# Kernel tuning notes

Hardware: AMD Instinct MI355X
Metric: run time of the kernel (lower is better)

## Reference

```python
import jax, jax.numpy as jnp
import numpy as np

B, S, V, D = 64, 256, 50000, 300
NW, CL, CV, CD = 8192, 16, 500, 30
H, T, CH = 128, 17, 30


def setup_inputs() -> dict:
    key = jax.random.key(0)
    ks = jax.random.split(key, 32)
    f32 = jnp.float32
    def rn(k, shape, scale=0.1):
        return jax.random.normal(k, shape, dtype=f32) * scale
    inp = {}
    inp["char_emb"] = rn(ks[0], (CV, CD)).at[0].set(0.0)  # padding_idx=0
    inp["conv_w"] = rn(ks[1], (CH, CD, 3))  # OIH
    inp["conv_b"] = rn(ks[2], (CH,))
    inp["word_emb"] = rn(ks[3], (V, D))
    in0, in1 = D + CH, 2 * H
    inp["w_ih_l0"] = rn(ks[4], (2, 3 * H, in0))  # [dir, 3H, in]
    inp["w_hh_l0"] = rn(ks[5], (2, 3 * H, H))
    inp["b_ih_l0"] = rn(ks[6], (2, 3 * H))
    inp["b_hh_l0"] = rn(ks[7], (2, 3 * H))
    inp["w_ih_l1"] = rn(ks[8], (2, 3 * H, in1))
    inp["w_hh_l1"] = rn(ks[9], (2, 3 * H, H))
    inp["b_ih_l1"] = rn(ks[10], (2, 3 * H))
    inp["b_hh_l1"] = rn(ks[11], (2, 3 * H))
    inp["mlp_w1"] = rn(ks[12], (2 * H, H))
    inp["mlp_b1"] = rn(ks[13], (H,))
    inp["mlp_w2"] = rn(ks[14], (H, T))
    inp["mlp_b2"] = rn(ks[15], (T,))
    inp["crf_start"] = rn(ks[16], (T,))
    inp["crf_end"] = rn(ks[17], (T,))
    inp["crf_trans"] = rn(ks[18], (T, T))
    inp["batched_char_words"] = jax.random.randint(ks[19], (NW, CL), 0, CV)
    inp["batched_char_words_len"] = jax.random.randint(ks[20], (NW,), 1, CL + 1)
    inp["batched_char_word_index"] = jax.random.randint(ks[21], (B, S), 0, NW + 1)
    inp["batched_tokens"] = jax.random.randint(ks[22], (B, S), 0, V)
    inp["batched_tokens_len"] = jax.random.randint(ks[23], (B,), S // 2, S + 1)
    inp["target"] = jax.random.randint(ks[24], (B, S), 0, T)
    return inp


def _gru_dir(x, mask, w_ih, w_hh, b_ih, b_hh, reverse):
    # x: [B,S,I], mask: [B,S] bool. Masked (padded) steps carry hidden state
    # through unchanged, matching pack_padded_sequence semantics.
    xg = jnp.einsum('bsi,gi->sbg', x, w_ih) + b_ih  # [S,B,3H]
    m = mask.T  # [S,B]
    h0 = jnp.zeros((x.shape[0], w_hh.shape[1]), x.dtype)

    def step(h, inp):
        xt, mt = inp
        hg = h @ w_hh.T + b_hh
        xr, xz, xn = jnp.split(xt, 3, axis=-1)
        hr, hz, hn = jnp.split(hg, 3, axis=-1)
        r = jax.nn.sigmoid(xr + hr)
        z = jax.nn.sigmoid(xz + hz)
        n = jnp.tanh(xn + r * hn)
        hnew = (1.0 - z) * n + z * h
        h = jnp.where(mt[:, None], hnew, h)
        return h, h

    _, hs = jax.lax.scan(step, h0, (xg, m), reverse=reverse)
    return hs.transpose(1, 0, 2)  # [B,S,H]


def _bigru_layer(x, mask, w_ih, w_hh, b_ih, b_hh):
    fwd = _gru_dir(x, mask, w_ih[0], w_hh[0], b_ih[0], b_hh[0], False)
    bwd = _gru_dir(x, mask, w_ih[1], w_hh[1], b_ih[1], b_hh[1], True)
    return jnp.concatenate([fwd, bwd], axis=-1)


def _forward(char_emb, conv_w, conv_b, word_emb,
             w_ih_l0, w_hh_l0, b_ih_l0, b_hh_l0,
             w_ih_l1, w_hh_l1, b_ih_l1, b_hh_l1,
             mlp_w1, mlp_b1, mlp_w2, mlp_b2,
             crf_start, crf_end, crf_trans,
             batched_char_words, batched_char_word_index,
             batched_tokens, batched_tokens_len, target):
    # --- char CNN token encoder: conv1d(k=3, SAME) + relu + max-over-time ---
    ct = char_emb[batched_char_words]  # [NW,CL,CD]
    c = jax.lax.conv_general_dilated(ct.transpose(0, 2, 1), conv_w, (1,), 'SAME',
                                     dimension_numbers=('NCH', 'OIH', 'NCH'))
    c = jax.nn.relu(c + conv_b[None, :, None])
    tok_enc = jnp.max(c, axis=-1)  # [NW,CH]
    tok_enc = jnp.concatenate([jnp.zeros((1, tok_enc.shape[1]), tok_enc.dtype), tok_enc], axis=0)
    tok_idx = tok_enc[batched_char_word_index]  # [B,S,CH] (index 0 -> zeros)

    texts = jnp.concatenate([word_emb[batched_tokens], tok_idx], axis=-1)  # [B,S,D+CH]
    seq = batched_tokens.shape[1]
    mask = jnp.arange(seq)[None, :] < batched_tokens_len[:, None]  # [B,S]

    # --- 2-layer BiGRU ---
    h = _bigru_layer(texts, mask, w_ih_l0, w_hh_l0, b_ih_l0, b_hh_l0)
    h = _bigru_layer(h, mask, w_ih_l1, w_hh_l1, b_ih_l1, b_hh_l1)

    # --- MLP head -> emissions [B,S,17] ---
    h = jax.nn.relu(h @ mlp_w1 + mlp_b1)
    emissions = h @ mlp_w2 + mlp_b2

    # --- CRF negative log-likelihood, reduction='token_mean' ---
    maskf = mask.astype(emissions.dtype)
    emit_sc = jnp.take_along_axis(emissions, target[..., None], axis=-1)[..., 0]  # [B,S]
    trans_sc = crf_trans[target[:, :-1], target[:, 1:]]  # [B,S-1]
    score = crf_start[target[:, 0]] + emit_sc[:, 0]
    score = score + jnp.sum((trans_sc + emit_sc[:, 1:]) * maskf[:, 1:], axis=1)
    last_tags = jnp.take_along_axis(target, (batched_tokens_len - 1)[:, None], axis=1)[:, 0]
    score = score + crf_end[last_tags]

    alpha0 = crf_start[None, :] + emissions[:, 0]  # [B,T]
    em_rest = emissions[:, 1:].transpose(1, 0, 2)  # [S-1,B,T]
    m_rest = mask[:, 1:].T  # [S-1,B]

    def crf_step(alpha, inp):
        emit, mt = inp
        new = jax.nn.logsumexp(alpha[:, :, None] + crf_trans[None], axis=1) + emit
        return jnp.where(mt[:, None], new, alpha), None

    alpha, _ = jax.lax.scan(crf_step, alpha0, (em_rest, m_rest))
    log_z = jax.nn.logsumexp(alpha + crf_end[None, :], axis=1)
    llh = score - log_z
    return -(jnp.sum(llh) / jnp.sum(maskf))


def reference(char_emb, conv_w, conv_b, word_emb,
              w_ih_l0, w_hh_l0, b_ih_l0, b_hh_l0,
              w_ih_l1, w_hh_l1, b_ih_l1, b_hh_l1,
              mlp_w1, mlp_b1, mlp_w2, mlp_b2,
              crf_start, crf_end, crf_trans,
              batched_char_words, batched_char_words_len,
              batched_char_word_index, batched_tokens, batched_tokens_len, target):
    return _forward(char_emb, conv_w, conv_b, word_emb,
                    w_ih_l0, w_hh_l0, b_ih_l0, b_hh_l0,
                    w_ih_l1, w_hh_l1, b_ih_l1, b_hh_l1,
                    mlp_w1, mlp_b1, mlp_w2, mlp_b2,
                    crf_start, crf_end, crf_trans,
                    batched_char_words, batched_char_word_index,
                    batched_tokens, batched_tokens_len, target)
```

## Files before the change

kernel.cpp:

```cpp
#include <hip/hip_runtime.h>
#include <cstddef>

#define BATCH 64
#define SEQ   256
#define VOCAB 50000
#define DIM   300
#define NW    8192
#define CLEN  16
#define CDIM  30
#define CHC   30
#define HID   128
#define NT    17
#define IN0   (DIM + CHC)
#define IN0P  336
#define IN1   (2 * HID)
#define NPOS  (BATCH * SEQ)

constexpr size_t SZ_XG    = 2ull * BATCH * SEQ * 384;
constexpr size_t SZ_TEXTS = (size_t)NPOS * IN0P;
constexpr size_t SZ_H1    = (size_t)NPOS * 256;
constexpr size_t SZ_TOK   = 245792;
constexpr size_t SZ_EMIS  = (size_t)NPOS * NT;
constexpr size_t SZ_WPAD  = 768ull * IN0P;
constexpr size_t OFF_XG    = 0;
constexpr size_t OFF_TEXTS = OFF_XG + SZ_XG;
constexpr size_t OFF_H1    = OFF_TEXTS + SZ_TEXTS;
constexpr size_t OFF_TOK   = OFF_H1 + SZ_H1;
constexpr size_t OFF_EMIS  = OFF_TOK + SZ_TOK;
constexpr size_t OFF_WPAD  = OFF_EMIS + SZ_EMIS;
constexpr size_t OFF_LLH   = OFF_WPAD + SZ_WPAD;

__device__ __forceinline__ float sigm(float x) {
    return 1.f / (1.f + __expf(-x));
}
__device__ __forceinline__ float tanh_fast(float x) {
    x = fminf(fmaxf(x, -15.f), 15.f);
    float e = __expf(-2.f * x);
    return (1.f - e) / (1.f + e);
}
__device__ __forceinline__ float oct_sum(float x) {
    int y = __builtin_amdgcn_update_dpp(0, __float_as_int(x), 0xB1, 0xF, 0xF, false);
    x += __int_as_float(y);
    y = __builtin_amdgcn_update_dpp(0, __float_as_int(x), 0x4E, 0xF, 0xF, false);
    x += __int_as_float(y);
    y = __builtin_amdgcn_update_dpp(0, __float_as_int(x), 0x141, 0xF, 0xF, false);
    x += __int_as_float(y);
    return x;
}

__global__ __launch_bounds__(256) void char_conv_k(
    const float* __restrict__ char_emb,
    const float* __restrict__ conv_w,
    const float* __restrict__ conv_b,
    const int*   __restrict__ words,
    float* __restrict__ tok_enc)
{
    __shared__ __align__(16) float cs[8][CLEN][CDIM];
    __shared__ float wsm[CHC * CDIM * 3];
    __shared__ float bs[CHC];
    int n0 = blockIdx.x * 8;
    int tid = threadIdx.x;
    for (int e = tid; e < CHC * CDIM * 3; e += 256) wsm[e] = conv_w[e];
    if (tid < CHC) bs[tid] = conv_b[tid];
    for (int e = tid; e < 8 * CLEN * CDIM; e += 256) {
        int wi = e / (CLEN * CDIM);
        int rem = e - wi * (CLEN * CDIM);
        int l = rem / CDIM;
        int i = rem - l * CDIM;
        int ci = words[(n0 + wi) * CLEN + l];
        cs[wi][l][i] = char_emb[ci * CDIM + i];
    }
    __syncthreads();
    int wi = tid >> 5;
    int o = tid & 31;
    if (o < CHC) {
        float best = -1e30f;
        for (int l = 0; l < CLEN; l++) {
            float s = 0.f;
            #pragma unroll
            for (int k = 0; k < 3; k++) {
                int ll = l + k - 1;
                if (ll >= 0 && ll < CLEN) {
                    #pragma unroll
                    for (int i = 0; i < CDIM; i++)
                        s += cs[wi][ll][i] * wsm[(o * CDIM + i) * 3 + k];
                }
            }
            best = fmaxf(best, s);
        }
        tok_enc[(size_t)(n0 + wi + 1) * CDIM + o] = fmaxf(best + bs[o], 0.f);
    }
}

__global__ __launch_bounds__(128) void build_texts_k(
    const float* __restrict__ word_emb,
    const float* __restrict__ tok_enc,
    const int*   __restrict__ tokens,
    const int*   __restrict__ widx,
    float* __restrict__ texts)
{
    int p = blockIdx.x;
    int tok = tokens[p];
    int ci = widx[p];
    float* o = texts + (size_t)p * IN0P;
    const float* wr = word_emb + (size_t)tok * DIM;
    const float* tr = tok_enc + (size_t)ci * CDIM;
    for (int c = threadIdx.x; c < IN0P; c += 128)
        o[c] = (c < DIM) ? wr[c] : (c < IN0 ? tr[c - DIM] : 0.f);
}

__global__ __launch_bounds__(64) void pad_w_k(
    const float* __restrict__ w, float* __restrict__ wp)
{
    int r = blockIdx.x;
    for (int c = threadIdx.x; c < IN0P; c += 64)
        wp[(size_t)r * IN0P + c] = (c < IN0) ? w[(size_t)r * IN0 + c] : 0.f;
}

#define GBM 128
#define GBN 128
#define GBK 16
__global__ __launch_bounds__(256) void gemm_xg_k(
    const float* __restrict__ A,
    const float* __restrict__ W,
    const float* __restrict__ bias,
    float* __restrict__ out,
    int K)
{
    __shared__ __align__(16) float As[GBK][GBM];
    __shared__ __align__(16) float Ws[GBK][GBN];
    int tid = threadIdx.x;
    int m0 = blockIdx.x * GBM;
    int n0 = blockIdx.y * GBN;
    int lrow = tid >> 1;
    int lk = (tid & 1) * 8;
    int ty = tid >> 4;
    int tx = tid & 15;

    float acc[8][8];
    #pragma unroll
    for (int i = 0; i < 8; i++)
        #pragma unroll
        for (int j = 0; j < 8; j++) acc[i][j] = 0.f;

    for (int k0 = 0; k0 < K; k0 += GBK) {
        const float4* ap = (const float4*)(A + (size_t)(m0 + lrow) * K + k0 + lk);
        const float4* wp = (const float4*)(W + (size_t)(n0 + lrow) * K + k0 + lk);
        float4 va0 = ap[0], va1 = ap[1];
        float4 vw0 = wp[0], vw1 = wp[1];
        As[lk + 0][lrow] = va0.x; As[lk + 1][lrow] = va0.y;
        As[lk + 2][lrow] = va0.z; As[lk + 3][lrow] = va0.w;
        As[lk + 4][lrow] = va1.x; As[lk + 5][lrow] = va1.y;
        As[lk + 6][lrow] = va1.z; As[lk + 7][lrow] = va1.w;
        Ws[lk + 0][lrow] = vw0.x; Ws[lk + 1][lrow] = vw0.y;
        Ws[lk + 2][lrow] = vw0.z; Ws[lk + 3][lrow] = vw0.w;
        Ws[lk + 4][lrow] = vw1.x; Ws[lk + 5][lrow] = vw1.y;
        Ws[lk + 6][lrow] = vw1.z; Ws[lk + 7][lrow] = vw1.w;
        __syncthreads();
        #pragma unroll
        for (int k = 0; k < GBK; k++) {
            float4 a0 = *(const float4*)&As[k][ty * 8];
            float4 a1 = *(const float4*)&As[k][ty * 8 + 4];
            float4 b0 = *(const float4*)&Ws[k][tx * 8];
            float4 b1 = *(const float4*)&Ws[k][tx * 8 + 4];
            float av[8] = {a0.x, a0.y, a0.z, a0.w, a1.x, a1.y, a1.z, a1.w};
            float bv[8] = {b0.x, b0.y, b0.z, b0.w, b1.x, b1.y, b1.z, b1.w};
            #pragma unroll
            for (int i = 0; i < 8; i++)
                #pragma unroll
                for (int j = 0; j < 8; j++)
                    acc[i][j] += av[i] * bv[j];
        }
        __syncthreads();
    }
    int nb = n0 + tx * 8;
    int d = nb / 384;
    int g0 = nb - d * 384;
    float bvv[8];
    #pragma unroll
    for (int j = 0; j < 8; j++) bvv[j] = bias[nb + j];
    int mbase = m0 + ty * 8;
    #pragma unroll
    for (int i = 0; i < 8; i++) {
        int m = mbase + i;
        int b = m >> 8;
        int t = m & 255;
        float* op = out + (((size_t)(d * BATCH + b) * SEQ + t) * 384 + g0);
        #pragma unroll
        for (int j = 0; j < 8; j++) op[j] = acc[i][j] + bvv[j];
    }
}

__global__ __launch_bounds__(512, 1) void gru_rec_k(
    const float* __restrict__ xg,
    const float* __restrict__ w_hh,
    const float* __restrict__ b_hh,
    const int*   __restrict__ lens,
    float* __restrict__ out)
{
    int d = blockIdx.x & 1;
    int b = blockIdx.x >> 1;
    int i = threadIdx.x;
    int e0 = i >> 3;
    int e1 = e0 + 64;
    int c = i & 7;
    __shared__ __align__(16) float hS[2][HID];

    const float* wb = w_hh + (size_t)d * 384 * HID;
    float4 wR0[4], wZ0[4], wN0[4], wR1[4], wZ1[4], wN1[4];
    #pragma unroll
    for (int q = 0; q < 4; q++) {
        int m = (q + c) & 3;
        int off = 16 * c + 4 * m;
        wR0[q] = *(const float4*)(wb + (size_t)(e0)       * HID + off);
        wZ0[q] = *(const float4*)(wb + (size_t)(128 + e0) * HID + off);
        wN0[q] = *(const float4*)(wb + (size_t)(256 + e0) * HID + off);
        wR1[q] = *(const float4*)(wb + (size_t)(e1)       * HID + off);
        wZ1[q] = *(const float4*)(wb + (size_t)(128 + e1) * HID + off);
        wN1[q] = *(const float4*)(wb + (size_t)(256 + e1) * HID + off);
    }
    float bhR0 = b_hh[d * 384 + e0];
    float bhZ0 = b_hh[d * 384 + 128 + e0];
    float bhN0 = b_hh[d * 384 + 256 + e0];
    float bhR1 = b_hh[d * 384 + e1];
    float bhZ1 = b_hh[d * 384 + 128 + e1];
    float bhN1 = b_hh[d * 384 + 256 + e1];
    int len = lens[b];

    if (i < HID) hS[0][i] = 0.f;
    float hold0 = 0.f, hold1 = 0.f;
    __syncthreads();

    const float* xgb = xg + ((size_t)(d * BATCH + b)) * SEQ * 384;
    float* outb = out + (size_t)b * SEQ * 256 + d * HID;

    int t0 = d ? (SEQ - 1) : 0;
    float xR0 = xgb[(size_t)t0 * 384 + e0];
    float xZ0 = xgb[(size_t)t0 * 384 + 128 + e0];
    float xN0 = xgb[(size_t)t0 * 384 + 256 + e0];
    float xR1 = xgb[(size_t)t0 * 384 + e1];
    float xZ1 = xgb[(size_t)t0 * 384 + 128 + e1];
    float xN1 = xgb[(size_t)t0 * 384 + 256 + e1];
    int tPrev = 0;

    for (int s = 0; s < SEQ; s++) {
        int t = d ? (SEQ - 1 - s) : s;
        if (s && c == 0) {
            outb[(size_t)tPrev * 256 + e0] = hold0;
            outb[(size_t)tPrev * 256 + e1] = hold1;
        }
        int sn = (s + 1 < SEQ) ? (s + 1) : s;
        int tn = d ? (SEQ - 1 - sn) : sn;
        float nxR0 = xgb[(size_t)tn * 384 + e0];
        float nxZ0 = xgb[(size_t)tn * 384 + 128 + e0];
        float nxN0 = xgb[(size_t)tn * 384 + 256 + e0];
        float nxR1 = xgb[(size_t)tn * 384 + e1];
        float nxZ1 = xgb[(size_t)tn * 384 + 128 + e1];
        float nxN1 = xgb[(size_t)tn * 384 + 256 + e1];

        const float4* hb = (const float4*)hS[s & 1] + 4 * c;
        float sR0 = 0.f, sZ0 = 0.f, sN0 = 0.f;
        float sR1 = 0.f, sZ1 = 0.f, sN1 = 0.f;
        #pragma unroll
        for (int q = 0; q < 4; q++) {
            int m = (q + c) & 3;
            float4 hv = hb[m];
            sR0 += wR0[q].x * hv.x + wR0[q].y * hv.y + wR0[q].z * hv.z + wR0[q].w * hv.w;
            sZ0 += wZ0[q].x * hv.x + wZ0[q].y * hv.y + wZ0[q].z * hv.z + wZ0[q].w * hv.w;
            sN0 += wN0[q].x * hv.x + wN0[q].y * hv.y + wN0[q].z * hv.z + wN0[q].w * hv.w;
            sR1 += wR1[q].x * hv.x + wR1[q].y * hv.y + wR1[q].z * hv.z + wR1[q].w * hv.w;
            sZ1 += wZ1[q].x * hv.x + wZ1[q].y * hv.y + wZ1[q].z * hv.z + wZ1[q].w * hv.w;
            sN1 += wN1[q].x * hv.x + wN1[q].y * hv.y + wN1[q].z * hv.z + wN1[q].w * hv.w;
        }
        sR0 = oct_sum(sR0); sZ0 = oct_sum(sZ0); sN0 = oct_sum(sN0);
        sR1 = oct_sum(sR1); sZ1 = oct_sum(sZ1); sN1 = oct_sum(sN1);

        float r0 = sigm(xR0 + sR0 + bhR0);
        float z0 = sigm(xZ0 + sZ0 + bhZ0);
        float n0 = tanh_fast(xN0 + r0 * (sN0 + bhN0));
        float hnew0 = (1.f - z0) * n0 + z0 * hold0;
        float r1 = sigm(xR1 + sR1 + bhR1);
        float z1 = sigm(xZ1 + sZ1 + bhZ1);
        float n1 = tanh_fast(xN1 + r1 * (sN1 + bhN1));
        float hnew1 = (1.f - z1) * n1 + z1 * hold1;
        bool upd = (t < len);
        hold0 = upd ? hnew0 : hold0;
        hold1 = upd ? hnew1 : hold1;
        if (c == 0) {
            hS[(s & 1) ^ 1][e0] = hold0;
            hS[(s & 1) ^ 1][e1] = hold1;
        }
        tPrev = t;
        xR0 = nxR0; xZ0 = nxZ0; xN0 = nxN0;
        xR1 = nxR1; xZ1 = nxZ1; xN1 = nxN1;
        __syncthreads();
    }
    if (c == 0) {
        outb[(size_t)tPrev * 256 + e0] = hold0;
        outb[(size_t)tPrev * 256 + e1] = hold1;
    }
}

__global__ __launch_bounds__(128) void mlp_emis_k(
    const float* __restrict__ h1,
    const float* __restrict__ w1,
    const float* __restrict__ b1,
    const float* __restrict__ w2,
    const float* __restrict__ b2,
    float* __restrict__ emis)
{
    __shared__ __align__(16) float hrow[8 * 256];
    __shared__ float hid[8][HID];
    int p0 = blockIdx.x * 8;
    int tid = threadIdx.x;
    for (int e = tid; e < 8 * 256; e += 128)
        hrow[e] = h1[(size_t)p0 * 256 + e];
    __syncthreads();
    float acc[8];
    float bb = b1[tid];
    #pragma unroll
    for (int i = 0; i < 8; i++) acc[i] = bb;
    for (int k = 0; k < 256; k++) {
        float wv = w1[k * HID + tid];
        #pragma unroll
        for (int i = 0; i < 8; i++) acc[i] += hrow[i * 256 + k] * wv;
    }
    #pragma unroll
    for (int i = 0; i < 8; i++) hid[i][tid] = fmaxf(acc[i], 0.f);
    __syncthreads();
    for (int idx = tid; idx < 8 * NT; idx += 128) {
        int pos = idx / NT;
        int tg = idx - pos * NT;
        float a = b2[tg];
        for (int k = 0; k < HID; k++) a += hid[pos][k] * w2[k * NT + tg];
        emis[(size_t)(p0 + pos) * NT + tg] = a;
    }
}

__global__ __launch_bounds__(64) void crf_k(
    const float* __restrict__ emis,
    const float* __restrict__ start,
    const float* __restrict__ endv,
    const float* __restrict__ trans,
    const int*   __restrict__ target,
    const int*   __restrict__ lens,
    float* __restrict__ llh)
{
    int b = blockIdx.x;
    int tid = threadIdx.x;
    __shared__ float tr[NT * NT];
    __shared__ float aSh[NT];
    __shared__ float scoreSh;
    for (int e = tid; e < NT * NT; e += 64) tr[e] = trans[e];
    __syncthreads();
    int len = lens[b];
    const int* tgt = target + b * SEQ;
    const float* eb = emis + (size_t)b * SEQ * NT;

    float part = 0.f;
    for (int t = 1 + tid; t < SEQ; t += 64) {
        if (t < len) {
            int tp = tgt[t - 1], tc = tgt[t];
            part += tr[tp * NT + tc] + eb[(size_t)t * NT + tc];
        }
    }
    #pragma unroll
    for (int off = 32; off > 0; off >>= 1)
        part += __shfl_down(part, off, 64);
    if (tid == 0) {
        int t0 = tgt[0];
        scoreSh = part + start[t0] + eb[t0] + endv[tgt[len - 1]];
    }

    float a = (tid < NT) ? (start[tid] + eb[tid]) : 0.f;
    for (int t = 1; t < SEQ; t++) {
        if (tid < NT) aSh[tid] = a;
        __syncthreads();
        if (t < len && tid < NT) {
            float m = -1e30f;
            #pragma unroll
            for (int i = 0; i < NT; i++)
                m = fmaxf(m, aSh[i] + tr[i * NT + tid]);
            float ssum = 0.f;
            #pragma unroll
            for (int i = 0; i < NT; i++)
                ssum += __expf(aSh[i] + tr[i * NT + tid] - m);
            a = m + __logf(ssum) + eb[(size_t)t * NT + tid];
        }
        __syncthreads();
    }
    float v = (tid < NT) ? (a + endv[tid]) : -1e30f;
    float m = v;
    #pragma unroll
    for (int off = 32; off > 0; off >>= 1)
        m = fmaxf(m, __shfl_down(m, off, 64));
    m = __shfl(m, 0, 64);
    float e = (tid < NT) ? __expf(v - m) : 0.f;
    #pragma unroll
    for (int off = 32; off > 0; off >>= 1)
        e += __shfl_down(e, off, 64);
    if (tid == 0) {
        float logz = m + __logf(e);
        llh[b] = scoreSh - logz;
    }
}

__global__ __launch_bounds__(64) void finalize_k(
    const float* __restrict__ llh,
    const int*   __restrict__ lens,
    float* __restrict__ out)
{
    int tid = threadIdx.x;
    float s = llh[tid];
    float lf = (float)lens[tid];
    #pragma unroll
    for (int off = 32; off > 0; off >>= 1) {
        s += __shfl_down(s, off, 64);
        lf += __shfl_down(lf, off, 64);
    }
    if (tid == 0) out[0] = -(s / lf);
}

extern "C" void kernel_launch(void* const* d_in, const int* in_sizes, int n_in,
                              void* d_out, int out_size, void* d_ws, size_t ws_size,
                              hipStream_t stream) {
    const float* char_emb = (const float*)d_in[0];
    const float* conv_w   = (const float*)d_in[1];
    const float* conv_b   = (const float*)d_in[2];
    const float* word_emb = (const float*)d_in[3];
    const float* w_ih_l0  = (const float*)d_in[4];
    const float* w_hh_l0  = (const float*)d_in[5];
    const float* b_ih_l0  = (const float*)d_in[6];
    const float* b_hh_l0  = (const float*)d_in[7];
    const float* w_ih_l1  = (const float*)d_in[8];
    const float* w_hh_l1  = (const float*)d_in[9];
    const float* b_ih_l1  = (const float*)d_in[10];
    const float* b_hh_l1  = (const float*)d_in[11];
    const float* mlp_w1   = (const float*)d_in[12];
    const float* mlp_b1   = (const float*)d_in[13];
    const float* mlp_w2   = (const float*)d_in[14];
    const float* mlp_b2   = (const float*)d_in[15];
    const float* crf_start= (const float*)d_in[16];
    const float* crf_end  = (const float*)d_in[17];
    const float* crf_trans= (const float*)d_in[18];
    const int* bcw   = (const int*)d_in[19];
    const int* bcwi  = (const int*)d_in[21];
    const int* btok  = (const int*)d_in[22];
    const int* blen  = (const int*)d_in[23];
    const int* target= (const int*)d_in[24];

    float* ws    = (float*)d_ws;
    float* xg    = ws + OFF_XG;
    float* texts = ws + OFF_TEXTS;
    float* h0    = texts;
    float* h1    = ws + OFF_H1;
    float* tok   = ws + OFF_TOK;
    float* emis  = ws + OFF_EMIS;
    float* wpad  = ws + OFF_WPAD;
    float* llh   = ws + OFF_LLH;

    hipMemsetAsync(tok, 0, CDIM * sizeof(float), stream);
    pad_w_k<<<768, 64, 0, stream>>>(w_ih_l0, wpad);
    char_conv_k<<<NW / 8, 256, 0, stream>>>(char_emb, conv_w, conv_b, bcw, tok);
    build_texts_k<<<NPOS, 128, 0, stream>>>(word_emb, tok, btok, bcwi, texts);
    gemm_xg_k<<<dim3(NPOS / GBM, 768 / GBN), 256, 0, stream>>>(texts, wpad, b_ih_l0, xg, IN0P);
    gru_rec_k<<<2 * BATCH, 512, 0, stream>>>(xg, w_hh_l0, b_hh_l0, blen, h0);
    gemm_xg_k<<<dim3(NPOS / GBM, 768 / GBN), 256, 0, stream>>>(h0, w_ih_l1, b_ih_l1, xg, IN1);
    gru_rec_k<<<2 * BATCH, 512, 0, stream>>>(xg, w_hh_l1, b_hh_l1, blen, h1);
    mlp_emis_k<<<NPOS / 8, 128, 0, stream>>>(h1, mlp_w1, mlp_b1, mlp_w2, mlp_b2, emis);
    crf_k<<<BATCH, 64, 0, stream>>>(emis, crf_start, crf_end, crf_trans, target, blen, llh);
    finalize_k<<<1, 64, 0, stream>>>(llh, blen, (float*)d_out);
}
```

Baseline: 1.017 ms.

## Restructure char conv with register weights and swizzle LDS to avoid bank conflicts

The char CNN now pads each character row to 32 floats and holds each channel's 90 weights in registers. It computes per-position partial sums for the three taps once, then combines neighbours, so the input rows are no longer reread for every tap. The xg GEMM pads its W tile and offsets columns to cut LDS bank conflicts on the float4 B-fragment reads. The GRU hidden-state buffer uses an XOR swizzle with a matching rotated access order to reduce LDS conflicts in the serial recurrence. The cost is higher register pressure in the conv kernel and more index arithmetic.

```diff
diff --git a/kernel.cpp b/kernel.cpp
--- a/kernel.cpp
+++ b/kernel.cpp
@@ -47,6 +47,7 @@
     x += __int_as_float(y);
     return x;
 }
+__device__ __forceinline__ int hswz(int j) { return j ^ ((j & 2) << 1); }
 
 __global__ __launch_bounds__(256) void char_conv_k(
     const float* __restrict__ char_emb,
@@ -55,37 +56,57 @@
     const int*   __restrict__ words,
     float* __restrict__ tok_enc)
 {
-    __shared__ __align__(16) float cs[8][CLEN][CDIM];
+    __shared__ __align__(16) float cs[8][CLEN][32];
     __shared__ float wsm[CHC * CDIM * 3];
     __shared__ float bs[CHC];
     int n0 = blockIdx.x * 8;
     int tid = threadIdx.x;
     for (int e = tid; e < CHC * CDIM * 3; e += 256) wsm[e] = conv_w[e];
     if (tid < CHC) bs[tid] = conv_b[tid];
-    for (int e = tid; e < 8 * CLEN * CDIM; e += 256) {
-        int wi = e / (CLEN * CDIM);
-        int rem = e - wi * (CLEN * CDIM);
-        int l = rem / CDIM;
-        int i = rem - l * CDIM;
-        int ci = words[(n0 + wi) * CLEN + l];
-        cs[wi][l][i] = char_emb[ci * CDIM + i];
+    for (int e = tid; e < 8 * CLEN * 32; e += 256) {
+        int wi = e >> 9;
+        int rem = e & 511;
+        int l = rem >> 5;
+        int ii = rem & 31;
+        float v = 0.f;
+        if (ii < CDIM) {
+            int ci = words[(n0 + wi) * CLEN + l];
+            v = char_emb[ci * CDIM + ii];
+        }
+        cs[wi][l][ii] = v;
     }
     __syncthreads();
     int wi = tid >> 5;
     int o = tid & 31;
     if (o < CHC) {
+        float wr[90];
+        #pragma unroll
+        for (int t = 0; t < 90; t++) wr[t] = wsm[o * 90 + t];
+        float P0[CLEN], P1[CLEN], P2[CLEN];
+        #pragma unroll
+        for (int l = 0; l < CLEN; l++) {
+            const float4* cr = (const float4*)cs[wi][l];
+            float s0 = 0.f, s1 = 0.f, s2 = 0.f;
+            #pragma unroll
+            for (int v4 = 0; v4 < 7; v4++) {
+                float4 cv = cr[v4];
+                int i0 = 4 * v4;
+                s0 += cv.x * wr[i0 * 3]     + cv.y * wr[(i0 + 1) * 3]     + cv.z * wr[(i0 + 2) * 3]     + cv.w * wr[(i0 + 3) * 3];
+                s1 += cv.x * wr[i0 * 3 + 1] + cv.y * wr[(i0 + 1) * 3 + 1] + cv.z * wr[(i0 + 2) * 3 + 1] + cv.w * wr[(i0 + 3) * 3 + 1];
+                s2 += cv.x * wr[i0 * 3 + 2] + cv.y * wr[(i0 + 1) * 3 + 2] + cv.z * wr[(i0 + 2) * 3 + 2] + cv.w * wr[(i0 + 3) * 3 + 2];
+            }
+            float4 cv7 = cr[7];
+            s0 += cv7.x * wr[84] + cv7.y * wr[87];
+            s1 += cv7.x * wr[85] + cv7.y * wr[88];
+            s2 += cv7.x * wr[86] + cv7.y * wr[89];
+            P0[l] = s0; P1[l] = s1; P2[l] = s2;
+        }
         float best = -1e30f;
-        for (int l = 0; l < CLEN; l++) {
-            float s = 0.f;
-            #pragma unroll
-            for (int k = 0; k < 3; k++) {
-                int ll = l + k - 1;
-                if (ll >= 0 && ll < CLEN) {
-                    #pragma unroll
-                    for (int i = 0; i < CDIM; i++)
-                        s += cs[wi][ll][i] * wsm[(o * CDIM + i) * 3 + k];
-                }
-            }
+        #pragma unroll
+        for (int lo = 0; lo < CLEN; lo++) {
+            float s = P1[lo];
+            if (lo > 0) s += P0[lo - 1];
+            if (lo < CLEN - 1) s += P2[lo + 1];
             best = fmaxf(best, s);
         }
         tok_enc[(size_t)(n0 + wi + 1) * CDIM + o] = fmaxf(best + bs[o], 0.f);
@@ -120,6 +141,7 @@
 #define GBM 128
 #define GBN 128
 #define GBK 16
+#define GBNP 132
 __global__ __launch_bounds__(256) void gemm_xg_k(
     const float* __restrict__ A,
     const float* __restrict__ W,
@@ -128,7 +150,7 @@
     int K)
 {
     __shared__ __align__(16) float As[GBK][GBM];
-    __shared__ __align__(16) float Ws[GBK][GBN];
+    __shared__ __align__(16) float Ws[GBK][GBNP];
     int tid = threadIdx.x;
     int m0 = blockIdx.x * GBM;
     int n0 = blockIdx.y * GBN;
@@ -136,6 +158,8 @@
     int lk = (tid & 1) * 8;
     int ty = tid >> 4;
     int tx = tid & 15;
+    int wcol = lrow + 4 * ((lrow >> 5) & 1);
+    int bbase = tx * 8 + 4 * ((tx >> 2) & 1);
 
     float acc[8][8];
     #pragma unroll
@@ -152,17 +176,17 @@
         As[lk + 2][lrow] = va0.z; As[lk + 3][lrow] = va0.w;
         As[lk + 4][lrow] = va1.x; As[lk + 5][lrow] = va1.y;
         As[lk + 6][lrow] = va1.z; As[lk + 7][lrow] = va1.w;
-        Ws[lk + 0][lrow] = vw0.x; Ws[lk + 1][lrow] = vw0.y;
-        Ws[lk + 2][lrow] = vw0.z; Ws[lk + 3][lrow] = vw0.w;
-        Ws[lk + 4][lrow] = vw1.x; Ws[lk + 5][lrow] = vw1.y;
-        Ws[lk + 6][lrow] = vw1.z; Ws[lk + 7][lrow] = vw1.w;
+        Ws[lk + 0][wcol] = vw0.x; Ws[lk + 1][wcol] = vw0.y;
+        Ws[lk + 2][wcol] = vw0.z; Ws[lk + 3][wcol] = vw0.w;
+        Ws[lk + 4][wcol] = vw1.x; Ws[lk + 5][wcol] = vw1.y;
+        Ws[lk + 6][wcol] = vw1.z; Ws[lk + 7][wcol] = vw1.w;
         __syncthreads();
         #pragma unroll
         for (int k = 0; k < GBK; k++) {
             float4 a0 = *(const float4*)&As[k][ty * 8];
             float4 a1 = *(const float4*)&As[k][ty * 8 + 4];
-            float4 b0 = *(const float4*)&Ws[k][tx * 8];
-            float4 b1 = *(const float4*)&Ws[k][tx * 8 + 4];
+            float4 b0 = *(const float4*)&Ws[k][bbase];
+            float4 b1 = *(const float4*)&Ws[k][bbase + 4];
             float av[8] = {a0.x, a0.y, a0.z, a0.w, a1.x, a1.y, a1.z, a1.w};
             float bv[8] = {b0.x, b0.y, b0.z, b0.w, b1.x, b1.y, b1.z, b1.w};
             #pragma unroll
@@ -210,7 +234,7 @@
     float4 wR0[4], wZ0[4], wN0[4], wR1[4], wZ1[4], wN1[4];
     #pragma unroll
     for (int q = 0; q < 4; q++) {
-        int m = (q + c) & 3;
+        int m = (q + (c >> 1)) & 3;
         int off = 16 * c + 4 * m;
         wR0[q] = *(const float4*)(wb + (size_t)(e0)       * HID + off);
         wZ0[q] = *(const float4*)(wb + (size_t)(128 + e0) * HID + off);
@@ -258,13 +282,14 @@
         float nxZ1 = xgb[(size_t)tn * 384 + 128 + e1];
         float nxN1 = xgb[(size_t)tn * 384 + 256 + e1];
 
-        const float4* hb = (const float4*)hS[s & 1] + 4 * c;
+        const float* hbase = hS[s & 1];
         float sR0 = 0.f, sZ0 = 0.f, sN0 = 0.f;
         float sR1 = 0.f, sZ1 = 0.f, sN1 = 0.f;
         #pragma unroll
         for (int q = 0; q < 4; q++) {
-            int m = (q + c) & 3;
-            float4 hv = hb[m];
+            int m = (q + (c >> 1)) & 3;
+            int j = 4 * c + m;
+            float4 hv = *(const float4*)(hbase + 4 * hswz(j));
             sR0 += wR0[q].x * hv.x + wR0[q].y * hv.y + wR0[q].z * hv.z + wR0[q].w * hv.w;
             sZ0 += wZ0[q].x * hv.x + wZ0[q].y * hv.y + wZ0[q].z * hv.z + wZ0[q].w * hv.w;
             sN0 += wN0[q].x * hv.x + wN0[q].y * hv.y + wN0[q].z * hv.z + wN0[q].w * hv.w;
@@ -287,8 +312,10 @@
         hold0 = upd ? hnew0 : hold0;
         hold1 = upd ? hnew1 : hold1;
         if (c == 0) {
-            hS[(s & 1) ^ 1][e0] = hold0;
-            hS[(s & 1) ^ 1][e1] = hold1;
+            float* hn = hS[(s & 1) ^ 1];
+            int j0 = e0 >> 2, j1 = e1 >> 2;
+            hn[4 * hswz(j0) + (e0 & 3)] = hold0;
+            hn[4 * hswz(j1) + (e1 & 3)] = hold1;
         }
         tPrev = t;
         xR0 = nxR0; xZ0 = nxZ0; xN0 = nxN0;
```

After: 1.029 ms. Within noise of the previous version (+1.2%).
